# Kernel optimization log

Hardware: AMD Instinct MI355X
Metric: run time of the kernel (lower is better)

The kernel has to match this reference:

```python
import jax, jax.numpy as jnp
import numpy as np

P, B, C, H, W = 8, 8, 64, 32, 32


def setup_inputs() -> dict:
    key = jax.random.key(0)
    k1, k2, k3 = jax.random.split(key, 3)
    shape = (P, B, C, H, W)
    return {
        "K_set": jax.random.normal(k1, shape, dtype=jnp.float32),
        "J_set": jax.random.normal(k2, shape, dtype=jnp.float32),
        "V_set": jax.random.normal(k3, shape, dtype=jnp.float32),
    }


def reference(K_set, J_set, V_set):
    # K_set/J_set/V_set: [P, B, C, H, W]; N = H*W spatial tokens.
    p, b, c, h, w = K_set.shape
    n = h * w
    Kf = K_set.reshape(p, b, c, n)  # [P,B,C,N]
    Jf = J_set.reshape(p, b, c, n)  # [P,B,C,N] (original permutes to [B,N,C])
    Vf = V_set.reshape(p, b, c, n)  # [P,B,C,N]
    # scores[p,b,j,k] = sum_c J[p,b,c,j] * K[p,b,c,k]  (unscaled QK^T)
    scores = jnp.einsum('pbcj,pbck->pbjk', Jf, Kf)
    # Original: F.softmax(bmm(J_pie, K_pie), dim=1) -> softmax over the J-token axis (j)
    att = jax.nn.softmax(scores, axis=2)
    # out[p,b,c,k] = sum_j V[p,b,c,j] * att[p,b,j,k]
    out = jnp.einsum('pbcj,pbjk->pbck', Vf, att)
    return out.reshape(p, b, c, h, w)
```

## Files before the change

### kernel.cpp

```cpp
#include <hip/hip_runtime.h>


typedef short bf16x8 __attribute__((ext_vector_type(8)));
typedef short bf16x4 __attribute__((ext_vector_type(4)));
typedef float f32x4  __attribute__((ext_vector_type(4)));

#define NTOK 1024
#define CH   64
#define KTW  128
#define JTILE 32
#define KW   32
#define SJK  72
#define SV   40

__device__ __forceinline__ unsigned short f2bf(float x) {
  unsigned int u = __float_as_uint(x);
  u += 0x7FFFu + ((u >> 16) & 1u);
  return (unsigned short)(u >> 16);
}
__device__ __forceinline__ float bf2f(unsigned short h) {
  return __uint_as_float(((unsigned int)h) << 16);
}

__global__ __launch_bounds__(256, 2) void attn_jk_softmax_v(
    const float* __restrict__ Kg, const float* __restrict__ Jg,
    const float* __restrict__ Vg, float* __restrict__ Og) {
  __shared__ unsigned short KhS[KTW][SJK];
  __shared__ unsigned short KlS[KTW][SJK];
  __shared__ unsigned short JhS[JTILE][SJK];
  __shared__ unsigned short JlS[JTILE][SJK];
  __shared__ unsigned short VtS[CH][SV];
  __shared__ unsigned short PtS[4][KW][SV];

  const int tid  = threadIdx.x;
  const int lane = tid & 63;
  const int wave = tid >> 6;
  const int l15  = lane & 15;
  const int l4   = lane >> 4;

  const int bid   = blockIdx.x;
  const int batch = bid & 63;
  const int ktile = bid >> 6;
  const int k0    = ktile * KTW;
  const size_t base = (size_t)batch * (CH * NTOK);

  const float* Kp = Kg + base;
  const float* Jp = Jg + base;
  const float* Vp = Vg + base;
  float*       Op = Og + base;

  #pragma unroll
  for (int i = 0; i < 4; ++i) {
    int task = i * 256 + tid;
    int k    = task & (KTW - 1);
    int oct  = task >> 7;
    const float* src = Kp + (size_t)(oct * 8) * NTOK + k0 + k;
    bf16x8 hv, lv;
    #pragma unroll
    for (int r = 0; r < 8; ++r) {
      float v = src[(size_t)r * NTOK];
      unsigned short h = f2bf(v);
      hv[r] = (short)h;
      lv[r] = (short)f2bf(v - bf2f(h));
    }
    *(bf16x8*)&KhS[k][oct * 8] = hv;
    *(bf16x8*)&KlS[k][oct * 8] = lv;
  }

  f32x4 U[4][2];
  #pragma unroll
  for (int a = 0; a < 4; ++a) {
    #pragma unroll
    for (int b = 0; b < 2; ++b) U[a][b] = (f32x4){0.f, 0.f, 0.f, 0.f};
  }
  float zacc0 = 0.f, zacc1 = 0.f;

  for (int jt = 0; jt < NTOK / JTILE; ++jt) {
    const int j0 = jt * JTILE;
    __syncthreads();

    {
      int j   = tid & 31;
      int oct = tid >> 5;
      const float* src = Jp + (size_t)(oct * 8) * NTOK + j0 + j;
      bf16x8 hv, lv;
      #pragma unroll
      for (int r = 0; r < 8; ++r) {
        float v = src[(size_t)r * NTOK];
        unsigned short h = f2bf(v);
        hv[r] = (short)h;
        lv[r] = (short)f2bf(v - bf2f(h));
      }
      *(bf16x8*)&JhS[j][oct * 8] = hv;
      *(bf16x8*)&JlS[j][oct * 8] = lv;
    }
    #pragma unroll
    for (int i = 0; i < 2; ++i) {
      int task = i * 256 + tid;
      int jq   = task & 7;
      int c    = task >> 3;
      const float4 v = *(const float4*)(Vp + (size_t)c * NTOK + j0 + jq * 4);
      bf16x4 pv;
      pv[0] = (short)f2bf(v.x); pv[1] = (short)f2bf(v.y);
      pv[2] = (short)f2bf(v.z); pv[3] = (short)f2bf(v.w);
      *(bf16x4*)&VtS[c][jq * 4] = pv;
    }
    __syncthreads();

    f32x4 S[2][2];
    #pragma unroll
    for (int a = 0; a < 2; ++a) {
      #pragma unroll
      for (int b = 0; b < 2; ++b) S[a][b] = (f32x4){0.f, 0.f, 0.f, 0.f};
    }
    #pragma unroll
    for (int cd = 0; cd < 2; ++cd) {
      const int co = cd * 32 + l4 * 8;
      bf16x8 ah0 = *(const bf16x8*)&JhS[l15][co];
      bf16x8 ah1 = *(const bf16x8*)&JhS[l15 + 16][co];
      bf16x8 al0 = *(const bf16x8*)&JlS[l15][co];
      bf16x8 al1 = *(const bf16x8*)&JlS[l15 + 16][co];
      bf16x8 bh0 = *(const bf16x8*)&KhS[wave * KW + l15][co];
      bf16x8 bh1 = *(const bf16x8*)&KhS[wave * KW + 16 + l15][co];
      bf16x8 bl0 = *(const bf16x8*)&KlS[wave * KW + l15][co];
      bf16x8 bl1 = *(const bf16x8*)&KlS[wave * KW + 16 + l15][co];
      S[0][0] = __builtin_amdgcn_mfma_f32_16x16x32_bf16(ah0, bh0, S[0][0], 0, 0, 0);
      S[0][0] = __builtin_amdgcn_mfma_f32_16x16x32_bf16(ah0, bl0, S[0][0], 0, 0, 0);
      S[0][0] = __builtin_amdgcn_mfma_f32_16x16x32_bf16(al0, bh0, S[0][0], 0, 0, 0);
      S[0][1] = __builtin_amdgcn_mfma_f32_16x16x32_bf16(ah0, bh1, S[0][1], 0, 0, 0);
      S[0][1] = __builtin_amdgcn_mfma_f32_16x16x32_bf16(ah0, bl1, S[0][1], 0, 0, 0);
      S[0][1] = __builtin_amdgcn_mfma_f32_16x16x32_bf16(al0, bh1, S[0][1], 0, 0, 0);
      S[1][0] = __builtin_amdgcn_mfma_f32_16x16x32_bf16(ah1, bh0, S[1][0], 0, 0, 0);
      S[1][0] = __builtin_amdgcn_mfma_f32_16x16x32_bf16(ah1, bl0, S[1][0], 0, 0, 0);
      S[1][0] = __builtin_amdgcn_mfma_f32_16x16x32_bf16(al1, bh0, S[1][0], 0, 0, 0);
      S[1][1] = __builtin_amdgcn_mfma_f32_16x16x32_bf16(ah1, bh1, S[1][1], 0, 0, 0);
      S[1][1] = __builtin_amdgcn_mfma_f32_16x16x32_bf16(ah1, bl1, S[1][1], 0, 0, 0);
      S[1][1] = __builtin_amdgcn_mfma_f32_16x16x32_bf16(al1, bh1, S[1][1], 0, 0, 0);
    }

    #pragma unroll
    for (int js = 0; js < 2; ++js) {
      #pragma unroll
      for (int ks = 0; ks < 2; ++ks) {
        f32x4 s = S[js][ks];
        float e0 = __expf(s[0]);
        float e1 = __expf(s[1]);
        float e2 = __expf(s[2]);
        float e3 = __expf(s[3]);
        if (ks == 0) zacc0 += (e0 + e1) + (e2 + e3);
        else         zacc1 += (e0 + e1) + (e2 + e3);
        bf16x4 pv;
        pv[0] = (short)f2bf(e0); pv[1] = (short)f2bf(e1);
        pv[2] = (short)f2bf(e2); pv[3] = (short)f2bf(e3);
        *(bf16x4*)&PtS[wave][l15 + ks * 16][js * 16 + l4 * 4] = pv;
      }
    }

    bf16x8 pb0 = *(const bf16x8*)&PtS[wave][l15][l4 * 8];
    bf16x8 pb1 = *(const bf16x8*)&PtS[wave][l15 + 16][l4 * 8];
    #pragma unroll
    for (int ct = 0; ct < 4; ++ct) {
      bf16x8 av = *(const bf16x8*)&VtS[ct * 16 + l15][l4 * 8];
      U[ct][0] = __builtin_amdgcn_mfma_f32_16x16x32_bf16(av, pb0, U[ct][0], 0, 0, 0);
      U[ct][1] = __builtin_amdgcn_mfma_f32_16x16x32_bf16(av, pb1, U[ct][1], 0, 0, 0);
    }
  }

  float z0 = zacc0; z0 += __shfl_xor(z0, 16); z0 += __shfl_xor(z0, 32);
  float z1 = zacc1; z1 += __shfl_xor(z1, 16); z1 += __shfl_xor(z1, 32);
  const float rz0 = 1.0f / z0;
  const float rz1 = 1.0f / z1;
  const int kbase = k0 + wave * KW;
  #pragma unroll
  for (int ct = 0; ct < 4; ++ct) {
    #pragma unroll
    for (int r = 0; r < 4; ++r) {
      int c = ct * 16 + l4 * 4 + r;
      Op[(size_t)c * NTOK + kbase + l15]      = U[ct][0][r] * rz0;
      Op[(size_t)c * NTOK + kbase + 16 + l15] = U[ct][1][r] * rz1;
    }
  }
}

extern "C" void kernel_launch(void* const* d_in, const int* in_sizes, int n_in,
                              void* d_out, int out_size, void* d_ws, size_t ws_size,
                              hipStream_t stream) {
  const float* Kg = (const float*)d_in[0];
  const float* Jg = (const float*)d_in[1];
  const float* Vg = (const float*)d_in[2];
  float* Og = (float*)d_out;
  attn_jk_softmax_v<<<dim3(512), dim3(256), 0, stream>>>(Kg, Jg, Vg, Og);
}
```

Baseline: 132.2 us.

## Prefetch next J/V tile into registers and hoist K fragments out of loop

Global loads for the next J/V tile are issued into registers before the current tile's MFMA work, so their latency overlaps compute (double-buffered registers, loop unrolled by two). The K hi/lo fragments are loaded from LDS once into registers instead of every iteration. The hi/lo bf16 split now uses truncation instead of round-to-nearest, which is cheaper but changes rounding of the split. The trade is higher register pressure under launch_bounds(256,2).

```diff
diff --git a/kernel.cpp b/kernel.cpp
--- a/kernel.cpp
+++ b/kernel.cpp
@@ -13,16 +13,15 @@
 #define SJK  72
 #define SV   40
 
-__device__ __forceinline__ unsigned short f2bf(float x) {
+__device__ __forceinline__ unsigned short f2bf_rne(float x) {
   unsigned int u = __float_as_uint(x);
   u += 0x7FFFu + ((u >> 16) & 1u);
   return (unsigned short)(u >> 16);
 }
-__device__ __forceinline__ float bf2f(unsigned short h) {
-  return __uint_as_float(((unsigned int)h) << 16);
-}
-
-__global__ __launch_bounds__(256, 2) void attn_jk_softmax_v(
+
+#define MFMA(a, b, c) __builtin_amdgcn_mfma_f32_16x16x32_bf16((a), (b), (c), 0, 0, 0)
+
+__global__ __launch_bounds__(256, 2) void attn_v2(
     const float* __restrict__ Kg, const float* __restrict__ Jg,
     const float* __restrict__ Vg, float* __restrict__ Og) {
   __shared__ unsigned short KhS[KTW][SJK];
@@ -59,13 +58,32 @@
     #pragma unroll
     for (int r = 0; r < 8; ++r) {
       float v = src[(size_t)r * NTOK];
-      unsigned short h = f2bf(v);
-      hv[r] = (short)h;
-      lv[r] = (short)f2bf(v - bf2f(h));
+      unsigned int u = __float_as_uint(v);
+      hv[r] = (short)(u >> 16);
+      float hf = __uint_as_float(u & 0xFFFF0000u);
+      lv[r] = (short)(__float_as_uint(v - hf) >> 16);
     }
     *(bf16x8*)&KhS[k][oct * 8] = hv;
     *(bf16x8*)&KlS[k][oct * 8] = lv;
   }
+  __syncthreads();
+
+  bf16x8 kbh[2][2], kbl[2][2];
+  #pragma unroll
+  for (int ks = 0; ks < 2; ++ks) {
+    #pragma unroll
+    for (int cd = 0; cd < 2; ++cd) {
+      kbh[ks][cd] = *(const bf16x8*)&KhS[wave * KW + ks * 16 + l15][cd * 32 + l4 * 8];
+      kbl[ks][cd] = *(const bf16x8*)&KlS[wave * KW + ks * 16 + l15][cd * 32 + l4 * 8];
+    }
+  }
+
+  const int jJ   = tid & 31;
+  const int octJ = tid >> 5;
+  const float* srcJ = Jp + (size_t)(octJ * 8) * NTOK + jJ;
+  const int c0  = tid >> 3;
+  const int jq0 = tid & 7;
+  const float* srcV = Vp + (size_t)c0 * NTOK + jq0 * 4;
 
   f32x4 U[4][2];
   #pragma unroll
@@ -75,38 +93,34 @@
   }
   float zacc0 = 0.f, zacc1 = 0.f;
 
-  for (int jt = 0; jt < NTOK / JTILE; ++jt) {
-    const int j0 = jt * JTILE;
-    __syncthreads();
-
-    {
-      int j   = tid & 31;
-      int oct = tid >> 5;
-      const float* src = Jp + (size_t)(oct * 8) * NTOK + j0 + j;
-      bf16x8 hv, lv;
-      #pragma unroll
-      for (int r = 0; r < 8; ++r) {
-        float v = src[(size_t)r * NTOK];
-        unsigned short h = f2bf(v);
-        hv[r] = (short)h;
-        lv[r] = (short)f2bf(v - bf2f(h));
-      }
-      *(bf16x8*)&JhS[j][oct * 8] = hv;
-      *(bf16x8*)&JlS[j][oct * 8] = lv;
-    }
-    #pragma unroll
-    for (int i = 0; i < 2; ++i) {
-      int task = i * 256 + tid;
-      int jq   = task & 7;
-      int c    = task >> 3;
-      const float4 v = *(const float4*)(Vp + (size_t)c * NTOK + j0 + jq * 4);
-      bf16x4 pv;
-      pv[0] = (short)f2bf(v.x); pv[1] = (short)f2bf(v.y);
-      pv[2] = (short)f2bf(v.z); pv[3] = (short)f2bf(v.w);
-      *(bf16x4*)&VtS[c][jq * 4] = pv;
-    }
-    __syncthreads();
-
+  auto issue_loads = [&](float (&jr)[8], float4 (&vr)[2], int j0) {
+    #pragma unroll
+    for (int r = 0; r < 8; ++r) jr[r] = srcJ[(size_t)r * NTOK + j0];
+    vr[0] = *(const float4*)(srcV + j0);
+    vr[1] = *(const float4*)(srcV + (size_t)32 * NTOK + j0);
+  };
+
+  auto stage = [&](float (&jr)[8], float4 (&vr)[2]) {
+    bf16x8 hv, lv;
+    #pragma unroll
+    for (int r = 0; r < 8; ++r) {
+      unsigned int u = __float_as_uint(jr[r]);
+      hv[r] = (short)(u >> 16);
+      float hf = __uint_as_float(u & 0xFFFF0000u);
+      lv[r] = (short)(__float_as_uint(jr[r] - hf) >> 16);
+    }
+    *(bf16x8*)&JhS[jJ][octJ * 8] = hv;
+    *(bf16x8*)&JlS[jJ][octJ * 8] = lv;
+    bf16x4 w0, w1;
+    w0[0] = (short)f2bf_rne(vr[0].x); w0[1] = (short)f2bf_rne(vr[0].y);
+    w0[2] = (short)f2bf_rne(vr[0].z); w0[3] = (short)f2bf_rne(vr[0].w);
+    w1[0] = (short)f2bf_rne(vr[1].x); w1[1] = (short)f2bf_rne(vr[1].y);
+    w1[2] = (short)f2bf_rne(vr[1].z); w1[3] = (short)f2bf_rne(vr[1].w);
+    *(bf16x4*)&VtS[c0][jq0 * 4]      = w0;
+    *(bf16x4*)&VtS[c0 + 32][jq0 * 4] = w1;
+  };
+
+  auto compute = [&]() {
     f32x4 S[2][2];
     #pragma unroll
     for (int a = 0; a < 2; ++a) {
@@ -120,24 +134,16 @@
       bf16x8 ah1 = *(const bf16x8*)&JhS[l15 + 16][co];
       bf16x8 al0 = *(const bf16x8*)&JlS[l15][co];
       bf16x8 al1 = *(const bf16x8*)&JlS[l15 + 16][co];
-      bf16x8 bh0 = *(const bf16x8*)&KhS[wave * KW + l15][co];
-      bf16x8 bh1 = *(const bf16x8*)&KhS[wave * KW + 16 + l15][co];
-      bf16x8 bl0 = *(const bf16x8*)&KlS[wave * KW + l15][co];
-      bf16x8 bl1 = *(const bf16x8*)&KlS[wave * KW + 16 + l15][co];
-      S[0][0] = __builtin_amdgcn_mfma_f32_16x16x32_bf16(ah0, bh0, S[0][0], 0, 0, 0);
-      S[0][0] = __builtin_amdgcn_mfma_f32_16x16x32_bf16(ah0, bl0, S[0][0], 0, 0, 0);
-      S[0][0] = __builtin_amdgcn_mfma_f32_16x16x32_bf16(al0, bh0, S[0][0], 0, 0, 0);
-      S[0][1] = __builtin_amdgcn_mfma_f32_16x16x32_bf16(ah0, bh1, S[0][1], 0, 0, 0);
-      S[0][1] = __builtin_amdgcn_mfma_f32_16x16x32_bf16(ah0, bl1, S[0][1], 0, 0, 0);
-      S[0][1] = __builtin_amdgcn_mfma_f32_16x16x32_bf16(al0, bh1, S[0][1], 0, 0, 0);
-      S[1][0] = __builtin_amdgcn_mfma_f32_16x16x32_bf16(ah1, bh0, S[1][0], 0, 0, 0);
-      S[1][0] = __builtin_amdgcn_mfma_f32_16x16x32_bf16(ah1, bl0, S[1][0], 0, 0, 0);
-      S[1][0] = __builtin_amdgcn_mfma_f32_16x16x32_bf16(al1, bh0, S[1][0], 0, 0, 0);
-      S[1][1] = __builtin_amdgcn_mfma_f32_16x16x32_bf16(ah1, bh1, S[1][1], 0, 0, 0);
-      S[1][1] = __builtin_amdgcn_mfma_f32_16x16x32_bf16(ah1, bl1, S[1][1], 0, 0, 0);
-      S[1][1] = __builtin_amdgcn_mfma_f32_16x16x32_bf16(al1, bh1, S[1][1], 0, 0, 0);
-    }
-
+      #pragma unroll
+      for (int ks = 0; ks < 2; ++ks) {
+        S[0][ks] = MFMA(ah0, kbh[ks][cd], S[0][ks]);
+        S[0][ks] = MFMA(ah0, kbl[ks][cd], S[0][ks]);
+        S[0][ks] = MFMA(al0, kbh[ks][cd], S[0][ks]);
+        S[1][ks] = MFMA(ah1, kbh[ks][cd], S[1][ks]);
+        S[1][ks] = MFMA(ah1, kbl[ks][cd], S[1][ks]);
+        S[1][ks] = MFMA(al1, kbh[ks][cd], S[1][ks]);
+      }
+    }
     #pragma unroll
     for (int js = 0; js < 2; ++js) {
       #pragma unroll
@@ -150,20 +156,41 @@
         if (ks == 0) zacc0 += (e0 + e1) + (e2 + e3);
         else         zacc1 += (e0 + e1) + (e2 + e3);
         bf16x4 pv;
-        pv[0] = (short)f2bf(e0); pv[1] = (short)f2bf(e1);
-        pv[2] = (short)f2bf(e2); pv[3] = (short)f2bf(e3);
+        pv[0] = (short)f2bf_rne(e0); pv[1] = (short)f2bf_rne(e1);
+        pv[2] = (short)f2bf_rne(e2); pv[3] = (short)f2bf_rne(e3);
         *(bf16x4*)&PtS[wave][l15 + ks * 16][js * 16 + l4 * 4] = pv;
       }
     }
-
     bf16x8 pb0 = *(const bf16x8*)&PtS[wave][l15][l4 * 8];
     bf16x8 pb1 = *(const bf16x8*)&PtS[wave][l15 + 16][l4 * 8];
     #pragma unroll
     for (int ct = 0; ct < 4; ++ct) {
       bf16x8 av = *(const bf16x8*)&VtS[ct * 16 + l15][l4 * 8];
-      U[ct][0] = __builtin_amdgcn_mfma_f32_16x16x32_bf16(av, pb0, U[ct][0], 0, 0, 0);
-      U[ct][1] = __builtin_amdgcn_mfma_f32_16x16x32_bf16(av, pb1, U[ct][1], 0, 0, 0);
-    }
+      U[ct][0] = MFMA(av, pb0, U[ct][0]);
+      U[ct][1] = MFMA(av, pb1, U[ct][1]);
+    }
+  };
+
+  float jrA[8], jrB[8];
+  float4 vrA[2], vrB[2];
+  issue_loads(jrA, vrA, 0);
+
+  #pragma unroll 1
+  for (int pr = 0; pr < NTOK / JTILE / 2; ++pr) {
+    __syncthreads();
+    stage(jrA, vrA);
+    __syncthreads();
+    issue_loads(jrB, vrB, (2 * pr + 1) * JTILE);
+    compute();
+
+    __syncthreads();
+    stage(jrB, vrB);
+    __syncthreads();
+    {
+      int jn = (2 * pr + 2 < NTOK / JTILE) ? (2 * pr + 2) * JTILE : 0;
+      issue_loads(jrA, vrA, jn);
+    }
+    compute();
   }
 
   float z0 = zacc0; z0 += __shfl_xor(z0, 16); z0 += __shfl_xor(z0, 32);
@@ -189,5 +216,5 @@
   const float* Jg = (const float*)d_in[1];
   const float* Vg = (const float*)d_in[2];
   float* Og = (float*)d_out;
-  attn_jk_softmax_v<<<dim3(512), dim3(256), 0, stream>>>(Kg, Jg, Vg, Og);
+  attn_v2<<<dim3(512), dim3(256), 0, stream>>>(Kg, Jg, Vg, Og);
 }
```

Measured after the change: 124.5 us. 1.06x faster.
